# Kernel tuning notes

Hardware: AMD Instinct MI355X
Metric: run time of the kernel (lower is better)

The kernel has to match this reference:

```python
import jax, jax.numpy as jnp
import numpy as np

PROB_THRESHOLD = 0.5  # default prob_threshold from the torch forward signature


def setup_inputs() -> dict:
    key = jax.random.key(0)
    mask = jax.random.uniform(key, (64, 512, 896), dtype=jnp.float32)  # per-pixel probabilities
    return {"mask": mask, "n_pts_threshold": 10, "dist_threshold": 64}


def rag_forward(mask, n_pts_threshold, dist_threshold, prob_threshold=PROB_THRESHOLD):
    # mask: [B, H, W] probability map.
    B, H, W = mask.shape
    binary = mask > prob_threshold                      # [B, H, W]
    n_pts = jnp.sum(binary, axis=(1, 2))                # [B] count of foreground points
    rows_any = jnp.any(binary, axis=2)                  # [B, H]
    cols_any = jnp.any(binary, axis=1)                  # [B, W]
    ridx = jnp.arange(H)
    cidx = jnp.arange(W)
    # Bounding box of foreground points (sentinels make empty rows/cols harmless).
    rmin = jnp.min(jnp.where(rows_any, ridx[None, :], H), axis=1)
    rmax = jnp.max(jnp.where(rows_any, ridx[None, :], -1), axis=1)
    cmin = jnp.min(jnp.where(cols_any, cidx[None, :], W), axis=1)
    cmax = jnp.max(jnp.where(cols_any, cidx[None, :], -1), axis=1)
    # Dilate box by dist_threshold and clip to image bounds.
    rmin = jnp.maximum(rmin - dist_threshold, 0)
    rmax = jnp.minimum(rmax + dist_threshold, H - 1)
    cmin = jnp.maximum(cmin - dist_threshold, 0)
    cmax = jnp.minimum(cmax + dist_threshold, W - 1)
    row_in = (ridx[None, :] >= rmin[:, None]) & (ridx[None, :] <= rmax[:, None])  # [B, H]
    col_in = (cidx[None, :] >= cmin[:, None]) & (cidx[None, :] <= cmax[:, None])  # [B, W]
    in_box = row_in[:, :, None] & col_in[:, None, :]                              # [B, H, W]
    # Too few confident points -> attend everywhere (all-ones map).
    enough = (n_pts >= n_pts_threshold)[:, None, None]
    att = jnp.where(enough, in_box, True).astype(mask.dtype)
    return att


def reference(mask, n_pts_threshold, dist_threshold):
    return rag_forward(mask, n_pts_threshold, dist_threshold)
```

## Files before the change

### kernel.cpp

```cpp
#include <hip/hip_runtime.h>

#define B 64
#define H 512
#define W 896
#define W4 (W / 4)
#define PIX (H * W)
#define VEC (PIX / 4)
#define TPB 256
#define SLICES 32
#define VEC_SLICE (VEC / SLICES)
#define ITERS (VEC_SLICE / TPB)
#define NBLK (B * SLICES)
#define PT 0.5f


__global__ __launch_bounds__(TPB) void rag_reduce_kernel(
        const float* __restrict__ mask, int* __restrict__ ws) {
    const int bid = blockIdx.x;
    const int b   = bid >> 5;
    const int tid = threadIdx.x;
    const int sbase = (bid & (SLICES - 1)) * VEC_SLICE + tid;

    const float4* m = reinterpret_cast<const float4*>(mask) + (size_t)b * VEC;

    int cnt = 0, rmn = H, rmx = -1, cmn = W, cmx = -1;

#pragma unroll
    for (int it = 0; it < ITERS; ++it) {
        const int i4 = sbase + it * TPB;
        const float4 v = m[i4];
        const bool f0 = v.x > PT;
        const bool f1 = v.y > PT;
        const bool f2 = v.z > PT;
        const bool f3 = v.w > PT;
        cnt += (int)f0 + (int)f1 + (int)f2 + (int)f3;
        if (f0 | f1 | f2 | f3) {
            const int row = i4 / W4;
            const int col = (i4 - row * W4) * 4;
            rmn = min(rmn, row);
            rmx = max(rmx, row);
            const int clo = f0 ? col : (f1 ? col + 1 : (f2 ? col + 2 : col + 3));
            const int chi = f3 ? col + 3 : (f2 ? col + 2 : (f1 ? col + 1 : col));
            cmn = min(cmn, clo);
            cmx = max(cmx, chi);
        }
    }

#pragma unroll
    for (int off = 32; off > 0; off >>= 1) {
        cnt += __shfl_down(cnt, off);
        rmn = min(rmn, __shfl_down(rmn, off));
        rmx = max(rmx, __shfl_down(rmx, off));
        cmn = min(cmn, __shfl_down(cmn, off));
        cmx = max(cmx, __shfl_down(cmx, off));
    }

    __shared__ int s[5][TPB / 64];
    const int wave = tid >> 6;
    if ((tid & 63) == 0) {
        s[0][wave] = cnt; s[1][wave] = rmn; s[2][wave] = rmx;
        s[3][wave] = cmn; s[4][wave] = cmx;
    }
    __syncthreads();
    if (tid == 0) {
#pragma unroll
        for (int wv = 1; wv < TPB / 64; ++wv) {
            cnt += s[0][wv];
            rmn = min(rmn, s[1][wv]);
            rmx = max(rmx, s[2][wv]);
            cmn = min(cmn, s[3][wv]);
            cmx = max(cmx, s[4][wv]);
        }
        ws[0 * NBLK + bid] = cnt;
        ws[1 * NBLK + bid] = rmn;
        ws[2 * NBLK + bid] = rmx;
        ws[3 * NBLK + bid] = cmn;
        ws[4 * NBLK + bid] = cmx;
    }
}

__global__ __launch_bounds__(TPB) void rag_fill_kernel(
        const int* __restrict__ ws,
        const int* __restrict__ nthr_p,
        const int* __restrict__ dthr_p,
        float* __restrict__ out) {
    const int bid = blockIdx.x;
    const int b   = bid >> 5;
    const int tid = threadIdx.x;

    __shared__ int sbox[4];
    if (tid < 64) {
        const int q = (b << 5) + (tid & 31);
        int c  = ws[0 * NBLK + q];
        int r0 = ws[1 * NBLK + q];
        int r1 = ws[2 * NBLK + q];
        int c0 = ws[3 * NBLK + q];
        int c1 = ws[4 * NBLK + q];
#pragma unroll
        for (int off = 16; off > 0; off >>= 1) {
            c  += __shfl_xor(c, off, 32);
            r0 = min(r0, __shfl_xor(r0, off, 32));
            r1 = max(r1, __shfl_xor(r1, off, 32));
            c0 = min(c0, __shfl_xor(c0, off, 32));
            c1 = max(c1, __shfl_xor(c1, off, 32));
        }
        if (tid == 0) {
            const int nthr = *nthr_p;
            const int dthr = *dthr_p;
            int brmn, brmx, bcmn, bcmx;
            if (c >= nthr) {
                brmn = max(r0 - dthr, 0);
                brmx = min(r1 + dthr, H - 1);
                bcmn = max(c0 - dthr, 0);
                bcmx = min(c1 + dthr, W - 1);
            } else {
                brmn = 0; brmx = H - 1; bcmn = 0; bcmx = W - 1;
            }
            sbox[0] = brmn; sbox[1] = brmx; sbox[2] = bcmn; sbox[3] = bcmx;
        }
    }
    __syncthreads();
    const int brmn = sbox[0], brmx = sbox[1], bcmn = sbox[2], bcmx = sbox[3];

    float4* ob = reinterpret_cast<float4*>(out) + (size_t)b * VEC;
    const int sbase = (bid & (SLICES - 1)) * VEC_SLICE + tid;

#pragma unroll
    for (int it = 0; it < ITERS; ++it) {
        const int i4 = sbase + it * TPB;
        const int row = i4 / W4;
        const int col = (i4 - row * W4) * 4;
        const bool rin = (row >= brmn) & (row <= brmx);
        float4 v;
        v.x = (rin & (col + 0 >= bcmn) & (col + 0 <= bcmx)) ? 1.0f : 0.0f;
        v.y = (rin & (col + 1 >= bcmn) & (col + 1 <= bcmx)) ? 1.0f : 0.0f;
        v.z = (rin & (col + 2 >= bcmn) & (col + 2 <= bcmx)) ? 1.0f : 0.0f;
        v.w = (rin & (col + 3 >= bcmn) & (col + 3 <= bcmx)) ? 1.0f : 0.0f;
        ob[i4] = v;
    }
}

extern "C" void kernel_launch(void* const* d_in, const int* in_sizes, int n_in,
                              void* d_out, int out_size, void* d_ws, size_t ws_size,
                              hipStream_t stream) {
    const float* mask = (const float*)d_in[0];
    const int*   nthr = (const int*)d_in[1];
    const int*   dthr = (const int*)d_in[2];
    float*       out  = (float*)d_out;
    int*         ws   = (int*)d_ws;

    rag_reduce_kernel<<<NBLK, TPB, 0, stream>>>(mask, ws);
    rag_fill_kernel<<<NBLK, TPB, 0, stream>>>(ws, nthr, dthr, out);
}
```

Baseline: 211.4 us.

## Fuse reduce and fill kernels with last-block election and spin-wait box broadcast

Merges the reduction and fill kernels into one launch. Each block publishes its partial stats and atomically bumps a per-batch counter. The last block of each batch reduces the partials and publishes the bounding box behind a release flag, while all blocks spin on that flag before writing their output slice. This removes the second kernel launch and the gap between the two kernels, but adds a memset launch and a spin-wait that depends on all blocks being co-resident. The MAGIC flag is never cleared between calls, so later calls can read a stale box from a previous invocation.

```diff
diff --git a/kernel.cpp b/kernel.cpp
--- a/kernel.cpp
+++ b/kernel.cpp
@@ -12,10 +12,17 @@
 #define ITERS (VEC_SLICE / TPB)
 #define NBLK (B * SLICES)
 #define PT 0.5f
+#define MAGIC 0x5A5A5A5A
 
+#define P_OFF 64
+#define X_OFF (P_OFF + 5 * NBLK)
 
-__global__ __launch_bounds__(TPB) void rag_reduce_kernel(
-        const float* __restrict__ mask, int* __restrict__ ws) {
+__global__ __launch_bounds__(TPB) void rag_fused_kernel(
+        const float* __restrict__ mask,
+        const int* __restrict__ nthr_p,
+        const int* __restrict__ dthr_p,
+        float* __restrict__ out,
+        int* __restrict__ ws) {
     const int bid = blockIdx.x;
     const int b   = bid >> 5;
     const int tid = threadIdx.x;
@@ -56,6 +63,8 @@
     }
 
     __shared__ int s[5][TPB / 64];
+    __shared__ int s_last;
+    __shared__ int sbox[4];
     const int wave = tid >> 6;
     if ((tid & 63) == 0) {
         s[0][wave] = cnt; s[1][wave] = rmn; s[2][wave] = rmx;
@@ -71,31 +80,23 @@
             cmn = min(cmn, s[3][wv]);
             cmx = max(cmx, s[4][wv]);
         }
-        ws[0 * NBLK + bid] = cnt;
-        ws[1 * NBLK + bid] = rmn;
-        ws[2 * NBLK + bid] = rmx;
-        ws[3 * NBLK + bid] = cmn;
-        ws[4 * NBLK + bid] = cmx;
+        __hip_atomic_store(&ws[P_OFF + 0 * NBLK + bid], cnt, __ATOMIC_RELAXED, __HIP_MEMORY_SCOPE_AGENT);
+        __hip_atomic_store(&ws[P_OFF + 1 * NBLK + bid], rmn, __ATOMIC_RELAXED, __HIP_MEMORY_SCOPE_AGENT);
+        __hip_atomic_store(&ws[P_OFF + 2 * NBLK + bid], rmx, __ATOMIC_RELAXED, __HIP_MEMORY_SCOPE_AGENT);
+        __hip_atomic_store(&ws[P_OFF + 3 * NBLK + bid], cmn, __ATOMIC_RELAXED, __HIP_MEMORY_SCOPE_AGENT);
+        __hip_atomic_store(&ws[P_OFF + 4 * NBLK + bid], cmx, __ATOMIC_RELAXED, __HIP_MEMORY_SCOPE_AGENT);
+        const int old = __hip_atomic_fetch_add(&ws[b], 1, __ATOMIC_ACQ_REL, __HIP_MEMORY_SCOPE_AGENT);
+        s_last = (old == SLICES - 1);
     }
-}
+    __syncthreads();
 
-__global__ __launch_bounds__(TPB) void rag_fill_kernel(
-        const int* __restrict__ ws,
-        const int* __restrict__ nthr_p,
-        const int* __restrict__ dthr_p,
-        float* __restrict__ out) {
-    const int bid = blockIdx.x;
-    const int b   = bid >> 5;
-    const int tid = threadIdx.x;
-
-    __shared__ int sbox[4];
-    if (tid < 64) {
-        const int q = (b << 5) + (tid & 31);
-        int c  = ws[0 * NBLK + q];
-        int r0 = ws[1 * NBLK + q];
-        int r1 = ws[2 * NBLK + q];
-        int c0 = ws[3 * NBLK + q];
-        int c1 = ws[4 * NBLK + q];
+    if (s_last && tid < 32) {
+        const int q = (b << 5) + tid;
+        int c  = __hip_atomic_load(&ws[P_OFF + 0 * NBLK + q], __ATOMIC_RELAXED, __HIP_MEMORY_SCOPE_AGENT);
+        int r0 = __hip_atomic_load(&ws[P_OFF + 1 * NBLK + q], __ATOMIC_RELAXED, __HIP_MEMORY_SCOPE_AGENT);
+        int r1 = __hip_atomic_load(&ws[P_OFF + 2 * NBLK + q], __ATOMIC_RELAXED, __HIP_MEMORY_SCOPE_AGENT);
+        int c0 = __hip_atomic_load(&ws[P_OFF + 3 * NBLK + q], __ATOMIC_RELAXED, __HIP_MEMORY_SCOPE_AGENT);
+        int c1 = __hip_atomic_load(&ws[P_OFF + 4 * NBLK + q], __ATOMIC_RELAXED, __HIP_MEMORY_SCOPE_AGENT);
 #pragma unroll
         for (int off = 16; off > 0; off >>= 1) {
             c  += __shfl_xor(c, off, 32);
@@ -116,15 +117,29 @@
             } else {
                 brmn = 0; brmx = H - 1; bcmn = 0; bcmx = W - 1;
             }
-            sbox[0] = brmn; sbox[1] = brmx; sbox[2] = bcmn; sbox[3] = bcmx;
+            int* box = &ws[X_OFF + b * 8];
+            __hip_atomic_store(&box[1], brmn, __ATOMIC_RELAXED, __HIP_MEMORY_SCOPE_AGENT);
+            __hip_atomic_store(&box[2], brmx, __ATOMIC_RELAXED, __HIP_MEMORY_SCOPE_AGENT);
+            __hip_atomic_store(&box[3], bcmn, __ATOMIC_RELAXED, __HIP_MEMORY_SCOPE_AGENT);
+            __hip_atomic_store(&box[4], bcmx, __ATOMIC_RELAXED, __HIP_MEMORY_SCOPE_AGENT);
+            __hip_atomic_store(&box[0], MAGIC, __ATOMIC_RELEASE, __HIP_MEMORY_SCOPE_AGENT);
         }
+    }
+
+    if (tid == 0) {
+        int* box = &ws[X_OFF + b * 8];
+        while (__hip_atomic_load(&box[0], __ATOMIC_ACQUIRE, __HIP_MEMORY_SCOPE_AGENT) != MAGIC) {
+            __builtin_amdgcn_s_sleep(2);
+        }
+        sbox[0] = __hip_atomic_load(&box[1], __ATOMIC_RELAXED, __HIP_MEMORY_SCOPE_AGENT);
+        sbox[1] = __hip_atomic_load(&box[2], __ATOMIC_RELAXED, __HIP_MEMORY_SCOPE_AGENT);
+        sbox[2] = __hip_atomic_load(&box[3], __ATOMIC_RELAXED, __HIP_MEMORY_SCOPE_AGENT);
+        sbox[3] = __hip_atomic_load(&box[4], __ATOMIC_RELAXED, __HIP_MEMORY_SCOPE_AGENT);
     }
     __syncthreads();
     const int brmn = sbox[0], brmx = sbox[1], bcmn = sbox[2], bcmx = sbox[3];
 
     float4* ob = reinterpret_cast<float4*>(out) + (size_t)b * VEC;
-    const int sbase = (bid & (SLICES - 1)) * VEC_SLICE + tid;
-
 #pragma unroll
     for (int it = 0; it < ITERS; ++it) {
         const int i4 = sbase + it * TPB;
@@ -149,6 +164,7 @@
     float*       out  = (float*)d_out;
     int*         ws   = (int*)d_ws;
 
-    rag_reduce_kernel<<<NBLK, TPB, 0, stream>>>(mask, ws);
-    rag_fill_kernel<<<NBLK, TPB, 0, stream>>>(ws, nthr, dthr, out);
+    hipMemsetAsync(ws, 0, B * sizeof(int), stream);
+
+    rag_fused_kernel<<<NBLK, TPB, 0, stream>>>(mask, nthr, dthr, out, ws);
 }
```

Measured after the change: 327.2 us. 1.55x slower.
